# Optimization experiments

Measured on AMD Instinct MI355X. Metric: run time of the kernel, lower is better.

Reference implementation:

```python
import jax, jax.numpy as jnp
import numpy as np


def setup_inputs() -> dict:
    key = jax.random.key(0)
    ks = jax.random.split(key, 4)
    B, T, M, E, F = 4, 2048, 1024, 8, 4096
    hidden_states = jax.random.normal(ks[0], (B, T, M), dtype=jnp.float32)
    wg = jax.random.normal(ks[1], (M, E), dtype=jnp.float32) * (1.0 / np.sqrt(M))
    w1 = jax.random.normal(ks[2], (E, M, F), dtype=jnp.float32) * (1.0 / np.sqrt(M))
    b1 = jnp.zeros((E, F), dtype=jnp.float32)
    w2 = jax.random.normal(ks[3], (E, F, M), dtype=jnp.float32) * (1.0 / np.sqrt(F))
    b2 = jnp.zeros((E, M), dtype=jnp.float32)
    return {"hidden_states": hidden_states, "wg": wg, "w1": w1, "b1": b1, "w2": w2, "b2": b2}


def reference(hidden_states, wg, w1, b1, w2, b2):
    B, T, M = hidden_states.shape
    E = wg.shape[1]
    S = B * T
    MIN_CAPACITY = 4
    C = max((S + E - 1) // E, MIN_CAPACITY)  # capacity_factor = 1 (static)

    x = hidden_states.reshape(S, M)  # [S, M]

    # --- top-1 gating (deepspeed TopKGate, noisy=None, use_rts=False) ---
    logits = x @ wg                                  # [S, E]
    gates = jax.nn.softmax(logits, axis=-1)          # [S, E]
    idx = jnp.argmax(gates, axis=-1)                 # [S]
    mask1 = jax.nn.one_hot(idx, E, dtype=gates.dtype)  # [S, E]
    # aux loss (computed before capacity drop)
    l_aux = jnp.sum(gates.mean(0) * mask1.mean(0)) * E
    # position of each token within its expert's queue
    locations1 = jnp.cumsum(mask1, axis=0) - 1.0     # [S, E]
    mask1 = mask1 * (locations1 < C)                 # drop overflow tokens
    gates1_s = jnp.sum(gates * mask1, axis=1)        # [S]
    loc_s = jnp.sum(locations1 * mask1, axis=1).astype(jnp.int32)  # [S]
    loc_sc = jax.nn.one_hot(loc_s, C, dtype=gates.dtype)           # [S, C]

    combine_weights = jnp.einsum('se,sc->sec', gates1_s[:, None] * mask1, loc_sc)  # [S,E,C]
    dispatch_mask = (combine_weights > 0).astype(x.dtype)

    # --- dispatch ---
    dispatched = jnp.einsum('sec,sm->ecm', dispatch_mask, x)  # [E, C, M]

    # --- expert FFN (grouped GEMM) ---
    h = jax.nn.gelu(jnp.einsum('ecm,emf->ecf', dispatched, w1) + b1[:, None, :])
    expert_out = jnp.einsum('ecf,efm->ecm', h, w2) + b2[:, None, :]  # [E, C, M]

    # --- combine ---
    out = jnp.einsum('sec,ecm->sm', combine_weights, expert_out)  # [S, M]
    return out.reshape(B, T, M)
```

## Files before the change

kernel.cpp:

```cpp
#include <hip/hip_runtime.h>
#include <hip/hip_bf16.h>
#include <math.h>

#define S_TOK 8192
#define M_DIM 1024
#define E_NUM 8
#define F_DIM 4096
#define CAP   1024

typedef short short8 __attribute__((ext_vector_type(8)));
typedef float f32x4 __attribute__((ext_vector_type(4)));
typedef unsigned short ushortx4 __attribute__((ext_vector_type(4)));

__device__ inline unsigned short f2bf(float f) {
    union { float f; unsigned int u; } v; v.f = f;
    unsigned int r = v.u + 0x7fffu + ((v.u >> 16) & 1u);
    return (unsigned short)(r >> 16);
}

__device__ inline float gelu_tanh(float x) {
    const float c = 0.7978845608028654f;
    float t = tanhf(c * (x + 0.044715f * x * x * x));
    return 0.5f * x * (1.0f + t);
}

__device__ inline void gl_lds16(const void* g, void* l) {
    __builtin_amdgcn_global_load_lds(
        (const __attribute__((address_space(1))) unsigned int*)g,
        (__attribute__((address_space(3))) unsigned int*)l, 16, 0, 0);
}

__global__ __launch_bounds__(256) void gating_kernel(
    const float* __restrict__ x, const float* __restrict__ wg,
    int* __restrict__ idx, float* __restrict__ gate)
{
    int wid = threadIdx.x >> 6;
    int lane = threadIdx.x & 63;
    int s = blockIdx.x * 4 + wid;
    const float* xs = x + (size_t)s * M_DIM;

    double acc[E_NUM];
#pragma unroll
    for (int e = 0; e < E_NUM; e++) acc[e] = 0.0;

    for (int i = lane; i < M_DIM; i += 64) {
        float xv = xs[i];
        float4 wa = *(const float4*)(wg + (size_t)i * E_NUM);
        float4 wb = *(const float4*)(wg + (size_t)i * E_NUM + 4);
        acc[0] += (double)xv * (double)wa.x;
        acc[1] += (double)xv * (double)wa.y;
        acc[2] += (double)xv * (double)wa.z;
        acc[3] += (double)xv * (double)wa.w;
        acc[4] += (double)xv * (double)wb.x;
        acc[5] += (double)xv * (double)wb.y;
        acc[6] += (double)xv * (double)wb.z;
        acc[7] += (double)xv * (double)wb.w;
    }
#pragma unroll
    for (int e = 0; e < E_NUM; e++) {
        double v = acc[e];
        for (int o = 32; o > 0; o >>= 1) v += __shfl_down(v, o, 64);
        acc[e] = v;
    }
    if (lane == 0) {
        double mx = acc[0]; int am = 0;
#pragma unroll
        for (int e = 1; e < E_NUM; e++) {
            if (acc[e] > mx) { mx = acc[e]; am = e; }
        }
        double se = 0.0;
#pragma unroll
        for (int e = 0; e < E_NUM; e++) se += exp(acc[e] - mx);
        idx[s] = am;
        gate[s] = (float)(1.0 / se);
    }
}

__global__ __launch_bounds__(1024) void scan_build(
    const int* __restrict__ idx, int* __restrict__ srcmap)
{
    __shared__ unsigned int sc[2][4][1024];
    int t = threadIdx.x;

    for (int i = t; i < E_NUM * CAP; i += 1024) srcmap[i] = -1;

    int eid[8];
    unsigned int cnt[E_NUM];
#pragma unroll
    for (int e = 0; e < E_NUM; e++) cnt[e] = 0;
#pragma unroll
    for (int i = 0; i < 8; i++) {
        int e = idx[t * 8 + i];
        eid[i] = e;
        cnt[e]++;
    }
    unsigned int pk[4];
#pragma unroll
    for (int i = 0; i < 4; i++) pk[i] = cnt[2 * i] | (cnt[2 * i + 1] << 16);
#pragma unroll
    for (int i = 0; i < 4; i++) sc[0][i][t] = pk[i];

    int buf = 0;
    for (int ofs = 1; ofs < 1024; ofs <<= 1) {
        __syncthreads();
        unsigned int v[4];
#pragma unroll
        for (int i = 0; i < 4; i++) {
            v[i] = sc[buf][i][t] + ((t >= ofs) ? sc[buf][i][t - ofs] : 0u);
            sc[buf ^ 1][i][t] = v[i];
        }
        buf ^= 1;
    }
    __syncthreads();
    unsigned int pos[E_NUM];
#pragma unroll
    for (int e = 0; e < E_NUM; e++) {
        unsigned int incl = (sc[buf][e >> 1][t] >> ((e & 1) * 16)) & 0xffffu;
        pos[e] = incl - cnt[e];
    }
#pragma unroll
    for (int i = 0; i < 8; i++) {
        int e = eid[i];
        unsigned int p = pos[e]++;
        if (p < CAP) srcmap[e * CAP + p] = t * 8 + i;
    }
}

__global__ __launch_bounds__(256) void dispatch_kernel(
    const float* __restrict__ x, const int* __restrict__ srcmap,
    unsigned short* __restrict__ A1)
{
    int slot = blockIdx.x;
    int s = srcmap[slot];
    int t = threadIdx.x;
    ushortx4 o;
    if (s >= 0) {
        float4 v = ((const float4*)(x + (size_t)s * M_DIM))[t];
        o[0] = f2bf(v.x); o[1] = f2bf(v.y); o[2] = f2bf(v.z); o[3] = f2bf(v.w);
    } else {
        o[0] = 0; o[1] = 0; o[2] = 0; o[3] = 0;
    }
    ((ushortx4*)(A1 + (size_t)slot * M_DIM))[t] = o;
}

__global__ __launch_bounds__(256) void transpose_cvt(
    const float* __restrict__ in, unsigned short* __restrict__ out, int R, int Cc)
{
    __shared__ float tile[32][33];
    int e = blockIdx.z;
    int br = blockIdx.y * 32, bc = blockIdx.x * 32;
    const float* ine = in + (size_t)e * R * Cc;
    unsigned short* oute = out + (size_t)e * R * Cc;
    int tx = threadIdx.x, ty = threadIdx.y;
#pragma unroll
    for (int i = 0; i < 32; i += 8)
        tile[ty + i][tx] = ine[(size_t)(br + ty + i) * Cc + (bc + tx)];
    __syncthreads();
#pragma unroll
    for (int i = 0; i < 32; i += 8)
        oute[(size_t)(bc + ty + i) * R + (br + tx)] = f2bf(tile[tx][ty + i]);
}

template <int MODE>
__global__ __launch_bounds__(256) void gemm_bf16(
    const unsigned short* __restrict__ A, const unsigned short* __restrict__ B,
    const float* __restrict__ bias, float* __restrict__ OutF,
    unsigned short* __restrict__ OutH,
    const int* __restrict__ srcmap, const float* __restrict__ gate,
    int K, int RA, int NB, int tilesM, int tilesN)
{
    __shared__ __align__(16) unsigned short As[128 * 32];
    __shared__ __align__(16) unsigned short Bs[128 * 32];

    int bid = blockIdx.x;
    int tpe = tilesM * tilesN;
    int e = bid / tpe;
    int rem = bid - e * tpe;
    int tm = rem / tilesN;
    int tn = rem - tm * tilesN;

    const unsigned short* Ae = A + ((size_t)e * RA + (size_t)tm * 128) * K;
    const unsigned short* Be = B + ((size_t)e * NB + (size_t)tn * 128) * K;

    int tid = threadIdx.x;
    int wid = tid >> 6, lane = tid & 63;
    int srow = wid * 32 + (lane >> 2);
    int schunk = (lane & 3) * 8;

    int fr = lane & 15, fk = (lane >> 4) * 8;
    int r0 = (wid >> 1) * 64, c0 = (wid & 1) * 64;

    f32x4 acc[4][4];
#pragma unroll
    for (int i = 0; i < 4; i++)
#pragma unroll
        for (int j = 0; j < 4; j++) acc[i][j] = (f32x4){0.f, 0.f, 0.f, 0.f};

    for (int k0 = 0; k0 < K; k0 += 32) {
        const unsigned short* ga = Ae + (size_t)srow * K + k0 + schunk;
        const unsigned short* gb = Be + (size_t)srow * K + k0 + schunk;
        gl_lds16(ga, &As[srow * 32 + schunk]);
        gl_lds16(ga + (size_t)16 * K, &As[(srow + 16) * 32 + schunk]);
        gl_lds16(gb, &Bs[srow * 32 + schunk]);
        gl_lds16(gb + (size_t)16 * K, &Bs[(srow + 16) * 32 + schunk]);
        asm volatile("s_waitcnt vmcnt(0)" ::: "memory");
        __syncthreads();

        short8 a[4], b[4];
#pragma unroll
        for (int mi = 0; mi < 4; mi++)
            a[mi] = *(const short8*)&As[(r0 + mi * 16 + fr) * 32 + fk];
#pragma unroll
        for (int ni = 0; ni < 4; ni++)
            b[ni] = *(const short8*)&Bs[(c0 + ni * 16 + fr) * 32 + fk];
#pragma unroll
        for (int mi = 0; mi < 4; mi++)
#pragma unroll
            for (int ni = 0; ni < 4; ni++)
                acc[mi][ni] = __builtin_amdgcn_mfma_f32_16x16x32_bf16(
                    a[mi], b[ni], acc[mi][ni], 0, 0, 0);
        __syncthreads();
    }

    int orow = (lane >> 4) * 4, ocol = lane & 15;
    if (MODE == 0) {
#pragma unroll
        for (int mi = 0; mi < 4; mi++) {
#pragma unroll
            for (int j = 0; j < 4; j++) {
                int r = tm * 128 + r0 + mi * 16 + orow + j;
                size_t rowbase = ((size_t)e * RA + r) * NB;
#pragma unroll
                for (int ni = 0; ni < 4; ni++) {
                    int c = tn * 128 + c0 + ni * 16 + ocol;
                    float v = acc[mi][ni][j] + bias[e * NB + c];
                    OutH[rowbase + c] = f2bf(gelu_tanh(v));
                }
            }
        }
    } else {
#pragma unroll
        for (int mi = 0; mi < 4; mi++) {
#pragma unroll
            for (int j = 0; j < 4; j++) {
                int r = tm * 128 + r0 + mi * 16 + orow + j;
                int slot = e * RA + r;
                int s = srcmap[slot];
                if (s < 0) continue;
                float g = gate[s];
                size_t rowbase = (size_t)s * NB;
#pragma unroll
                for (int ni = 0; ni < 4; ni++) {
                    int c = tn * 128 + c0 + ni * 16 + ocol;
                    OutF[rowbase + c] = g * (acc[mi][ni][j] + bias[e * NB + c]);
                }
            }
        }
    }
}

extern "C" void kernel_launch(void* const* d_in, const int* in_sizes, int n_in,
                              void* d_out, int out_size, void* d_ws, size_t ws_size,
                              hipStream_t stream) {
    const float* x  = (const float*)d_in[0];
    const float* wg = (const float*)d_in[1];
    const float* w1 = (const float*)d_in[2];
    const float* b1 = (const float*)d_in[3];
    const float* w2 = (const float*)d_in[4];
    const float* b2 = (const float*)d_in[5];
    float* out = (float*)d_out;

    char* ws = (char*)d_ws;
    unsigned short* A1  = (unsigned short*)(ws);
    unsigned short* W1T = (unsigned short*)(ws + (size_t)(16u << 20));
    unsigned short* W2T = (unsigned short*)(ws + (size_t)(80u << 20));
    unsigned short* H   = (unsigned short*)(ws + (size_t)(144u << 20));
    int*   idx  = (int*)(ws + (size_t)(208u << 20));
    float* gate = (float*)(ws + (size_t)(208u << 20) + 32768);
    int*   srcm = (int*)(ws + (size_t)(208u << 20) + 65536);

    hipMemsetAsync(d_out, 0, (size_t)S_TOK * M_DIM * sizeof(float), stream);

    gating_kernel<<<S_TOK / 4, 256, 0, stream>>>(x, wg, idx, gate);
    scan_build<<<1, 1024, 0, stream>>>(idx, srcm);
    dispatch_kernel<<<E_NUM * CAP, 256, 0, stream>>>(x, srcm, A1);
    transpose_cvt<<<dim3(F_DIM / 32, M_DIM / 32, E_NUM), dim3(32, 8), 0, stream>>>(
        w1, W1T, M_DIM, F_DIM);
    transpose_cvt<<<dim3(M_DIM / 32, F_DIM / 32, E_NUM), dim3(32, 8), 0, stream>>>(
        w2, W2T, F_DIM, M_DIM);

    gemm_bf16<0><<<E_NUM * (CAP / 128) * (F_DIM / 128), 256, 0, stream>>>(
        A1, W1T, b1, nullptr, H, nullptr, nullptr,
        M_DIM, CAP, F_DIM, CAP / 128, F_DIM / 128);

    gemm_bf16<1><<<E_NUM * (CAP / 128) * (M_DIM / 128), 256, 0, stream>>>(
        H, W2T, b2, out, nullptr, srcm, gate,
        F_DIM, CAP, M_DIM, CAP / 128, M_DIM / 128);
}
```

Measured before the change: 396.0 us.

## Double-buffer LDS tiles in grouped GEMM and use exp2-based GELU

The grouped bf16 GEMM now uses two LDS buffers per operand. The next K-slice is fetched with global_load_lds while MFMAs run on the current slice, so global-load latency can overlap compute and one barrier per iteration is dropped. The tanh-based GELU is replaced with an algebraically equivalent x*sigmoid(2y) form computed via exp2f, to make the epilogue cheaper. The change doubles LDS use, which may reduce occupancy, and the fast GELU may differ slightly numerically.

New measurement: 375.8 us. -5.1%, faster.

```diff
diff --git a/kernel.cpp b/kernel.cpp
--- a/kernel.cpp
+++ b/kernel.cpp
@@ -18,10 +18,11 @@
     return (unsigned short)(r >> 16);
 }
 
-__device__ inline float gelu_tanh(float x) {
-    const float c = 0.7978845608028654f;
-    float t = tanhf(c * (x + 0.044715f * x * x * x));
-    return 0.5f * x * (1.0f + t);
+__device__ inline float gelu_fast(float x) {
+    float y = 0.7978845608028654f * (x + 0.044715f * x * x * x);
+    if (y > 40.f) return x;
+    float e = exp2f(2.8853900817779268f * y);
+    return x * e / (e + 1.0f);
 }
 
 __device__ inline void gl_lds16(const void* g, void* l) {
@@ -169,8 +170,8 @@
     const int* __restrict__ srcmap, const float* __restrict__ gate,
     int K, int RA, int NB, int tilesM, int tilesN)
 {
-    __shared__ __align__(16) unsigned short As[128 * 32];
-    __shared__ __align__(16) unsigned short Bs[128 * 32];
+    __shared__ __align__(16) unsigned short As[2][128 * 32];
+    __shared__ __align__(16) unsigned short Bs[2][128 * 32];
 
     int bid = blockIdx.x;
     int tpe = tilesM * tilesN;
@@ -190,37 +191,48 @@
     int fr = lane & 15, fk = (lane >> 4) * 8;
     int r0 = (wid >> 1) * 64, c0 = (wid & 1) * 64;
 
+#define STAGE(bufi, kk) do {                                                  \
+    const unsigned short* ga = Ae + (size_t)srow * K + (kk) + schunk;         \
+    const unsigned short* gb = Be + (size_t)srow * K + (kk) + schunk;         \
+    gl_lds16(ga,                 &As[bufi][srow * 32 + schunk]);              \
+    gl_lds16(ga + (size_t)16 * K, &As[bufi][(srow + 16) * 32 + schunk]);      \
+    gl_lds16(gb,                 &Bs[bufi][srow * 32 + schunk]);              \
+    gl_lds16(gb + (size_t)16 * K, &Bs[bufi][(srow + 16) * 32 + schunk]);      \
+} while (0)
+
     f32x4 acc[4][4];
 #pragma unroll
     for (int i = 0; i < 4; i++)
 #pragma unroll
         for (int j = 0; j < 4; j++) acc[i][j] = (f32x4){0.f, 0.f, 0.f, 0.f};
 
+    STAGE(0, 0);
+    asm volatile("s_waitcnt vmcnt(0)" ::: "memory");
+    __syncthreads();
+
+    int cur = 0;
     for (int k0 = 0; k0 < K; k0 += 32) {
-        const unsigned short* ga = Ae + (size_t)srow * K + k0 + schunk;
-        const unsigned short* gb = Be + (size_t)srow * K + k0 + schunk;
-        gl_lds16(ga, &As[srow * 32 + schunk]);
-        gl_lds16(ga + (size_t)16 * K, &As[(srow + 16) * 32 + schunk]);
-        gl_lds16(gb, &Bs[srow * 32 + schunk]);
-        gl_lds16(gb + (size_t)16 * K, &Bs[(srow + 16) * 32 + schunk]);
-        asm volatile("s_waitcnt vmcnt(0)" ::: "memory");
-        __syncthreads();
+        if (k0 + 32 < K) STAGE(cur ^ 1, k0 + 32);
 
         short8 a[4], b[4];
 #pragma unroll
         for (int mi = 0; mi < 4; mi++)
-            a[mi] = *(const short8*)&As[(r0 + mi * 16 + fr) * 32 + fk];
+            a[mi] = *(const short8*)&As[cur][(r0 + mi * 16 + fr) * 32 + fk];
 #pragma unroll
         for (int ni = 0; ni < 4; ni++)
-            b[ni] = *(const short8*)&Bs[(c0 + ni * 16 + fr) * 32 + fk];
+            b[ni] = *(const short8*)&Bs[cur][(c0 + ni * 16 + fr) * 32 + fk];
 #pragma unroll
         for (int mi = 0; mi < 4; mi++)
 #pragma unroll
             for (int ni = 0; ni < 4; ni++)
                 acc[mi][ni] = __builtin_amdgcn_mfma_f32_16x16x32_bf16(
                     a[mi], b[ni], acc[mi][ni], 0, 0, 0);
+
+        asm volatile("s_waitcnt vmcnt(0)" ::: "memory");
         __syncthreads();
-    }
+        cur ^= 1;
+    }
+#undef STAGE
 
     int orow = (lane >> 4) * 4, ocol = lane & 15;
     if (MODE == 0) {
@@ -234,7 +246,7 @@
                 for (int ni = 0; ni < 4; ni++) {
                     int c = tn * 128 + c0 + ni * 16 + ocol;
                     float v = acc[mi][ni][j] + bias[e * NB + c];
-                    OutH[rowbase + c] = f2bf(gelu_tanh(v));
+                    OutH[rowbase + c] = f2bf(gelu_fast(v));
                 }
             }
         }
```
